# Optimization experiments

Measured on AMD Instinct MI355X. Metric: run time of the kernel, lower is better.

## Reference

```python
import jax, jax.numpy as jnp
import numpy as np

WH, WW = 7, 7
L = WH * WW            # 49 tokens per window
C = 128                # embedding dim
H = 32                 # heads
HD = C // H            # head dim = 4
BN = 4096              # batch * num_windows


def _relative_position_index(wh, ww):
    coords = np.stack(np.meshgrid(np.arange(wh), np.arange(ww), indexing='ij'))  # [2,wh,ww]
    flat = coords.reshape(2, -1)                     # [2, L]
    rel = flat[:, :, None] - flat[:, None, :]        # [2, L, L]
    rel = rel.transpose(1, 2, 0).copy()              # [L, L, 2]
    rel[:, :, 0] += wh - 1
    rel[:, :, 1] += ww - 1
    rel[:, :, 0] *= 2 * ww - 1
    return jnp.asarray(rel.sum(-1), dtype=jnp.int32)  # [L, L]


REL_IDX = _relative_position_index(WH, WW)


def setup_inputs() -> dict:
    key = jax.random.key(0)
    k1, k2, k3, k4 = jax.random.split(key, 4)
    x = jax.random.normal(k1, (BN, L, C), dtype=jnp.float32)
    W_qkv = jax.random.normal(k2, (C, 3 * C), dtype=jnp.float32) * (C ** -0.5)
    b_qkv = jnp.zeros((3 * C,), dtype=jnp.float32)
    W_proj = jax.random.normal(k3, (C, C), dtype=jnp.float32) * (C ** -0.5)
    b_proj = jnp.zeros((C,), dtype=jnp.float32)
    bias_table = jax.random.normal(k4, ((2 * WH - 1) * (2 * WW - 1), H), dtype=jnp.float32) * 0.02
    return {"x": x, "W_qkv": W_qkv, "b_qkv": b_qkv, "W_proj": W_proj,
            "b_proj": b_proj, "bias_table": bias_table}


def reference(x, W_qkv, b_qkv, W_proj, b_proj, bias_table):
    bn, l, c = x.shape
    scale = HD ** -0.5
    qkv = x @ W_qkv + b_qkv                                   # [BN, L, 3C]
    qkv = qkv.reshape(bn, l, 3, H, HD).transpose(2, 0, 3, 1, 4)  # [3, BN, H, L, HD]
    q, k, v = qkv[0], qkv[1], qkv[2]
    attn = jnp.einsum('bhqd,bhkd->bhqk', q * scale, k)        # [BN, H, L, L]
    rel_bias = bias_table[REL_IDX]                            # [L, L, H]
    attn = attn + rel_bias.transpose(2, 0, 1)[None]           # add [1, H, L, L]
    attn = jax.nn.softmax(attn, axis=-1)
    out = jnp.einsum('bhqk,bhkd->bhqd', attn, v)              # [BN, H, L, HD]
    out = out.transpose(0, 2, 1, 3).reshape(bn, l, c)         # [BN, L, C]
    return out @ W_proj + b_proj
```

## Files before the change

kernel.cpp:

```cpp
#include <hip/hip_runtime.h>
#include <hip/hip_bf16.h>
#include <stdint.h>

#define L 49
#define C 128
#define H 32

typedef __attribute__((ext_vector_type(8))) short bf16x8;
typedef __attribute__((ext_vector_type(4))) float f32x4;

#define XP 136
#define VTP 72
#define QKP 264

#define LOG2E 1.44269504f

__device__ __forceinline__ uint32_t rbits(float f) {
  return __builtin_bit_cast(uint32_t, f) + 0x8000u;
}
__device__ __forceinline__ uint32_t pack2(float a, float b) {
  return __builtin_amdgcn_perm(rbits(b), rbits(a), 0x07060302u);
}
__device__ __forceinline__ ushort bf1(float a) { return (ushort)(rbits(a) >> 16); }

__device__ __forceinline__ bf16x8 mk_frag(uint2 d, bool valid) {
  union { uint32_t u[4]; bf16x8 v; } r;
  r.u[0] = valid ? d.x : 0u;
  r.u[1] = valid ? d.y : 0u;
  r.u[2] = 0u; r.u[3] = 0u;
  return r.v;
}
__device__ __forceinline__ bf16x8 zero8() {
  union { uint32_t u[4]; bf16x8 v; } r;
  r.u[0] = r.u[1] = r.u[2] = r.u[3] = 0u;
  return r.v;
}
__device__ __forceinline__ bf16x8 ones8() {
  union { uint32_t u[4]; bf16x8 v; } r;
  r.u[0] = r.u[1] = r.u[2] = r.u[3] = 0x3F803F80u;
  return r.v;
}

__global__ void __launch_bounds__(256) prep_weights_kernel(
    const float* __restrict__ Wqkv, const float* __restrict__ Wproj,
    ushort* __restrict__ ws) {
  int i = blockIdx.x * 256 + threadIdx.x;
  if (i < 384 * 128) {
    int n = i >> 7, k = i & 127;
    ws[i] = bf1(Wqkv[k * 384 + n]);
  } else {
    int j = i - 384 * 128;
    if (j < 128 * 128) {
      int n = j >> 7, k = j & 127;
      ws[49152 + j] = bf1(Wproj[k * 128 + n]);
    }
  }
}

__global__ void __launch_bounds__(256) prep_bias_kernel(
    const float* __restrict__ bt, float* __restrict__ biasx) {
  int i = blockIdx.x * 256 + threadIdx.x;
  int r = i & 3, lane = (i >> 2) & 63, t = i >> 8;
  int nt = t & 3, mt = (t >> 2) & 3, h = t >> 4;
  int q = nt * 16 + (lane & 15);
  int k = mt * 16 + ((lane >> 4) & 3) * 4 + r;
  float v = -1e30f;
  if (q < L && k < L) {
    int qi = q / 7, qj = q % 7, ki = k / 7, kj = k % 7;
    int idx = (qi - ki + 6) * 13 + (qj - kj + 6);
    v = bt[idx * H + h] * LOG2E;
  }
  biasx[i] = v;
}

__global__ void __launch_bounds__(256, 3) win_attn_kernel(
    const float* __restrict__ x,
    const float* __restrict__ b_qkv,
    const float* __restrict__ b_proj,
    const ushort* __restrict__ wqkvT,
    const ushort* __restrict__ wprojT,
    const float* __restrict__ biasx,
    float* __restrict__ out) {
  __shared__ alignas(16) ushort s_xv[C * VTP];
  __shared__ alignas(16) ushort qk[L * QKP];
  __shared__ alignas(16) ushort p_lds[4][16 * 64];

  ushort* xa = s_xv;
  ushort* vt = s_xv;

  const int tid = threadIdx.x;
  const int w = blockIdx.x;
  const int wv = tid >> 6;
  const int l = tid & 63;
  const int lr = l & 15;
  const int lg = l >> 4;

  {
    const float4* xv = (const float4*)(x + (size_t)w * (L * C));
    for (int i = tid; i < L * C / 4; i += 256) {
      float4 v = xv[i];
      int e = i * 4;
      int r = e >> 7, c = e & 127;
      uint2 u = make_uint2(pack2(v.x, v.y), pack2(v.z, v.w));
      *(uint2*)&xa[r * XP + c] = u;
    }
  }
  __syncthreads();

  {
    bf16x8 af[4][4];
    #pragma unroll
    for (int mt = 0; mt < 4; ++mt) {
      int row = mt * 16 + lr; if (row > 48) row = 48;
      #pragma unroll
      for (int kk = 0; kk < 4; ++kk)
        af[mt][kk] = *(const bf16x8*)&xa[row * XP + kk * 32 + lg * 8];
    }
    __syncthreads();
    for (int ntl = 0; ntl < 6; ++ntl) {
      int nt = wv * 6 + ntl;
      int ncol = nt * 16 + lr;
      const ushort* bp = wqkvT + ncol * C + lg * 8;
      bf16x8 b0 = *(const bf16x8*)(bp);
      bf16x8 b1 = *(const bf16x8*)(bp + 32);
      bf16x8 b2 = *(const bf16x8*)(bp + 64);
      bf16x8 b3 = *(const bf16x8*)(bp + 96);
      float bias = b_qkv[ncol];
      float sc = (ncol < 128) ? 0.5f * LOG2E : 1.0f;
      #pragma unroll
      for (int mt = 0; mt < 4; ++mt) {
        f32x4 acc = {0.f, 0.f, 0.f, 0.f};
        acc = __builtin_amdgcn_mfma_f32_16x16x32_bf16(af[mt][0], b0, acc, 0, 0, 0);
        acc = __builtin_amdgcn_mfma_f32_16x16x32_bf16(af[mt][1], b1, acc, 0, 0, 0);
        acc = __builtin_amdgcn_mfma_f32_16x16x32_bf16(af[mt][2], b2, acc, 0, 0, 0);
        acc = __builtin_amdgcn_mfma_f32_16x16x32_bf16(af[mt][3], b3, acc, 0, 0, 0);
        if (ncol < 256) {
          #pragma unroll
          for (int r = 0; r < 4; ++r) {
            int row = mt * 16 + lg * 4 + r;
            if (row < L) qk[row * QKP + ncol] = bf1((acc[r] + bias) * sc);
          }
        } else {
          int kbase = mt * 16 + lg * 4;
          uint2 pv = make_uint2(pack2(acc[0] + bias, acc[1] + bias),
                                pack2(acc[2] + bias, acc[3] + bias));
          *(uint2*)&vt[(ncol - 256) * VTP + kbase] = pv;
        }
      }
    }
  }
  __syncthreads();

  {
    char* pw = (char*)&p_lds[wv][0];
    #pragma unroll 1
    for (int hh = 0; hh < 8; ++hh) {
      int h = wv * 8 + hh;
      f32x4 acc[4][4];
      #pragma unroll
      for (int mt = 0; mt < 4; ++mt)
        #pragma unroll
        for (int nt = 0; nt < 4; ++nt)
          acc[mt][nt] = ((const f32x4*)biasx)[(h * 16 + mt * 4 + nt) * 64 + l];
      bf16x8 ka[4], qb[4];
      #pragma unroll
      for (int mt = 0; mt < 4; ++mt) {
        int row = mt * 16 + lr; if (row > 48) row = 48;
        uint2 d = *(const uint2*)&qk[row * QKP + 128 + h * 4];
        ka[mt] = mk_frag(d, lg == 0);
      }
      #pragma unroll
      for (int nt = 0; nt < 4; ++nt) {
        int row = nt * 16 + lr; if (row > 48) row = 48;
        uint2 d = *(const uint2*)&qk[row * QKP + h * 4];
        qb[nt] = mk_frag(d, lg == 0);
      }
      #pragma unroll
      for (int nt = 0; nt < 4; ++nt)
        #pragma unroll
        for (int mt = 0; mt < 4; ++mt)
          acc[mt][nt] = __builtin_amdgcn_mfma_f32_16x16x32_bf16(ka[mt], qb[nt], acc[mt][nt], 0, 0, 0);
      bf16x8 va[2];
      #pragma unroll
      for (int ks = 0; ks < 2; ++ks) {
        bf16x8 t = *(const bf16x8*)&vt[(h * 4 + (lr & 3)) * VTP + ks * 32 + lg * 8];
        va[ks] = (lr < 4) ? t : ((lr == 4) ? ones8() : zero8());
      }
      #pragma unroll
      for (int nt = 0; nt < 4; ++nt) {
        #pragma unroll
        for (int mt = 0; mt < 4; ++mt) {
          uint32_t u0 = rbits(__builtin_amdgcn_exp2f(acc[mt][nt][0]));
          uint32_t u1 = rbits(__builtin_amdgcn_exp2f(acc[mt][nt][1]));
          uint32_t u2 = rbits(__builtin_amdgcn_exp2f(acc[mt][nt][2]));
          uint32_t u3 = rbits(__builtin_amdgcn_exp2f(acc[mt][nt][3]));
          uint32_t d0 = __builtin_amdgcn_perm(u1, u0, 0x07060302u);
          uint32_t d1 = __builtin_amdgcn_perm(u3, u2, 0x07060302u);
          int byte = lr * 128 + mt * 32 + lg * 8;
          byte ^= (lr & 7) << 4;
          *(uint2*)(pw + byte) = make_uint2(d0, d1);
        }
        f32x4 oo = {0.f, 0.f, 0.f, 0.f};
        #pragma unroll
        for (int ks = 0; ks < 2; ++ks) {
          int byte = lr * 128 + ks * 64 + lg * 16;
          byte ^= (lr & 7) << 4;
          bf16x8 pb = *(const bf16x8*)(pw + byte);
          oo = __builtin_amdgcn_mfma_f32_16x16x32_bf16(va[ks], pb, oo, 0, 0, 0);
        }
        float den = __shfl_xor(oo[0], 16);
        if (lg == 0) {
          float iv = __builtin_amdgcn_rcpf(den);
          int q = nt * 16 + lr;
          if (q < L) {
            uint2 od = make_uint2(pack2(oo[0] * iv, oo[1] * iv),
                                  pack2(oo[2] * iv, oo[3] * iv));
            *(uint2*)&qk[q * QKP + h * 4] = od;
          }
        }
      }
    }
  }
  __syncthreads();

  {
    bf16x8 pf[4][4];
    #pragma unroll
    for (int mt = 0; mt < 4; ++mt) {
      int row = mt * 16 + lr; if (row > 48) row = 48;
      #pragma unroll
      for (int kk = 0; kk < 4; ++kk)
        pf[mt][kk] = *(const bf16x8*)&qk[row * QKP + kk * 32 + lg * 8];
    }
    float* outw = out + (size_t)w * (L * C);
    for (int ntl = 0; ntl < 2; ++ntl) {
      int ncol = (wv * 2 + ntl) * 16 + lr;
      const ushort* bp = wprojT + ncol * C + lg * 8;
      bf16x8 b0 = *(const bf16x8*)(bp);
      bf16x8 b1 = *(const bf16x8*)(bp + 32);
      bf16x8 b2 = *(const bf16x8*)(bp + 64);
      bf16x8 b3 = *(const bf16x8*)(bp + 96);
      float bias = b_proj[ncol];
      #pragma unroll
      for (int mt = 0; mt < 4; ++mt) {
        f32x4 acc = {0.f, 0.f, 0.f, 0.f};
        acc = __builtin_amdgcn_mfma_f32_16x16x32_bf16(pf[mt][0], b0, acc, 0, 0, 0);
        acc = __builtin_amdgcn_mfma_f32_16x16x32_bf16(pf[mt][1], b1, acc, 0, 0, 0);
        acc = __builtin_amdgcn_mfma_f32_16x16x32_bf16(pf[mt][2], b2, acc, 0, 0, 0);
        acc = __builtin_amdgcn_mfma_f32_16x16x32_bf16(pf[mt][3], b3, acc, 0, 0, 0);
        #pragma unroll
        for (int r = 0; r < 4; ++r) {
          int row = mt * 16 + lg * 4 + r;
          if (row < L) outw[row * C + ncol] = acc[r] + bias;
        }
      }
    }
  }
}

extern "C" void kernel_launch(void* const* d_in, const int* in_sizes, int n_in,
                              void* d_out, int out_size, void* d_ws, size_t ws_size,
                              hipStream_t stream) {
  const float* x     = (const float*)d_in[0];
  const float* Wqkv  = (const float*)d_in[1];
  const float* bqkv  = (const float*)d_in[2];
  const float* Wproj = (const float*)d_in[3];
  const float* bproj = (const float*)d_in[4];
  const float* btab  = (const float*)d_in[5];
  float* out = (float*)d_out;
  ushort* ws = (ushort*)d_ws;
  float* biasx = (float*)(ws + 65536);

  int bn = in_sizes[0] / (L * C);

  hipLaunchKernelGGL(prep_weights_kernel, dim3(256), dim3(256), 0, stream,
                     Wqkv, Wproj, ws);
  hipLaunchKernelGGL(prep_bias_kernel, dim3(512), dim3(256), 0, stream,
                     btab, biasx);
  hipLaunchKernelGGL(win_attn_kernel, dim3(bn), dim3(256), 0, stream,
                     x, bqkv, bproj, ws, ws + 49152, biasx, out);
}
```

Measured before the change: 195.5 us.

## Double-buffer per-head bias loads and raise MFMA priority in attention loop

Splits the per-head attention loop into pairs of heads with two accumulator sets, so the relative-bias loads for the next head are issued while the current head computes. MFMA sections are wrapped in s_setprio to favour matrix issue across waves, and the QKV and projection column loops get an unroll-by-2 hint. The aim is to hide global bias-load latency behind compute. The second accumulator set doubles accumulator registers, which risks spills or lower occupancy under the 3-blocks-per-CU launch bound.

```diff
diff --git a/kernel.cpp b/kernel.cpp
--- a/kernel.cpp
+++ b/kernel.cpp
@@ -73,6 +73,72 @@
   biasx[i] = v;
 }
 
+__device__ __forceinline__ void head_body(
+    f32x4 (&acc)[4][4], int h, const ushort* qk, const ushort* vt,
+    char* pw, ushort* qk_mut, int lr, int lg) {
+  bf16x8 ka[4], qb[4];
+  #pragma unroll
+  for (int mt = 0; mt < 4; ++mt) {
+    int row = mt * 16 + lr; if (row > 48) row = 48;
+    uint2 d = *(const uint2*)&qk[row * QKP + 128 + h * 4];
+    ka[mt] = mk_frag(d, lg == 0);
+  }
+  #pragma unroll
+  for (int nt = 0; nt < 4; ++nt) {
+    int row = nt * 16 + lr; if (row > 48) row = 48;
+    uint2 d = *(const uint2*)&qk[row * QKP + h * 4];
+    qb[nt] = mk_frag(d, lg == 0);
+  }
+  __builtin_amdgcn_s_setprio(1);
+  #pragma unroll
+  for (int nt = 0; nt < 4; ++nt)
+    #pragma unroll
+    for (int mt = 0; mt < 4; ++mt)
+      acc[mt][nt] = __builtin_amdgcn_mfma_f32_16x16x32_bf16(ka[mt], qb[nt], acc[mt][nt], 0, 0, 0);
+  __builtin_amdgcn_s_setprio(0);
+  bf16x8 va[2];
+  #pragma unroll
+  for (int ks = 0; ks < 2; ++ks) {
+    bf16x8 t = *(const bf16x8*)&vt[(h * 4 + (lr & 3)) * VTP + ks * 32 + lg * 8];
+    va[ks] = (lr < 4) ? t : ((lr == 4) ? ones8() : zero8());
+  }
+  #pragma unroll
+  for (int nt = 0; nt < 4; ++nt) {
+    #pragma unroll
+    for (int mt = 0; mt < 4; ++mt) {
+      uint32_t u0 = rbits(__builtin_amdgcn_exp2f(acc[mt][nt][0]));
+      uint32_t u1 = rbits(__builtin_amdgcn_exp2f(acc[mt][nt][1]));
+      uint32_t u2 = rbits(__builtin_amdgcn_exp2f(acc[mt][nt][2]));
+      uint32_t u3 = rbits(__builtin_amdgcn_exp2f(acc[mt][nt][3]));
+      uint32_t d0 = __builtin_amdgcn_perm(u1, u0, 0x07060302u);
+      uint32_t d1 = __builtin_amdgcn_perm(u3, u2, 0x07060302u);
+      int byte = lr * 128 + mt * 32 + lg * 8;
+      byte ^= (lr & 7) << 4;
+      *(uint2*)(pw + byte) = make_uint2(d0, d1);
+    }
+    f32x4 oo = {0.f, 0.f, 0.f, 0.f};
+    __builtin_amdgcn_s_setprio(1);
+    #pragma unroll
+    for (int ks = 0; ks < 2; ++ks) {
+      int byte = lr * 128 + ks * 64 + lg * 16;
+      byte ^= (lr & 7) << 4;
+      bf16x8 pb = *(const bf16x8*)(pw + byte);
+      oo = __builtin_amdgcn_mfma_f32_16x16x32_bf16(va[ks], pb, oo, 0, 0, 0);
+    }
+    __builtin_amdgcn_s_setprio(0);
+    float den = __shfl_xor(oo[0], 16);
+    if (lg == 0) {
+      float iv = __builtin_amdgcn_rcpf(den);
+      int q = nt * 16 + lr;
+      if (q < L) {
+        uint2 od = make_uint2(pack2(oo[0] * iv, oo[1] * iv),
+                              pack2(oo[2] * iv, oo[3] * iv));
+        *(uint2*)&qk_mut[q * QKP + h * 4] = od;
+      }
+    }
+  }
+}
+
 __global__ void __launch_bounds__(256, 3) win_attn_kernel(
     const float* __restrict__ x,
     const float* __restrict__ b_qkv,
@@ -117,6 +183,7 @@
         af[mt][kk] = *(const bf16x8*)&xa[row * XP + kk * 32 + lg * 8];
     }
     __syncthreads();
+    #pragma unroll 2
     for (int ntl = 0; ntl < 6; ++ntl) {
       int nt = wv * 6 + ntl;
       int ncol = nt * 16 + lr;
@@ -153,72 +220,33 @@
 
   {
     char* pw = (char*)&p_lds[wv][0];
+    const f32x4* bx = (const f32x4*)biasx;
+    const int hbase = wv * 8;
+
+    f32x4 accA[4][4], accB[4][4];
+    #pragma unroll
+    for (int mt = 0; mt < 4; ++mt)
+      #pragma unroll
+      for (int nt = 0; nt < 4; ++nt)
+        accA[mt][nt] = bx[(hbase * 16 + mt * 4 + nt) * 64 + l];
+
     #pragma unroll 1
-    for (int hh = 0; hh < 8; ++hh) {
-      int h = wv * 8 + hh;
-      f32x4 acc[4][4];
+    for (int hp = 0; hp < 4; ++hp) {
+      int h0 = hbase + hp * 2;
       #pragma unroll
       for (int mt = 0; mt < 4; ++mt)
         #pragma unroll
         for (int nt = 0; nt < 4; ++nt)
-          acc[mt][nt] = ((const f32x4*)biasx)[(h * 16 + mt * 4 + nt) * 64 + l];
-      bf16x8 ka[4], qb[4];
-      #pragma unroll
-      for (int mt = 0; mt < 4; ++mt) {
-        int row = mt * 16 + lr; if (row > 48) row = 48;
-        uint2 d = *(const uint2*)&qk[row * QKP + 128 + h * 4];
-        ka[mt] = mk_frag(d, lg == 0);
-      }
-      #pragma unroll
-      for (int nt = 0; nt < 4; ++nt) {
-        int row = nt * 16 + lr; if (row > 48) row = 48;
-        uint2 d = *(const uint2*)&qk[row * QKP + h * 4];
-        qb[nt] = mk_frag(d, lg == 0);
-      }
-      #pragma unroll
-      for (int nt = 0; nt < 4; ++nt)
+          accB[mt][nt] = bx[((h0 + 1) * 16 + mt * 4 + nt) * 64 + l];
+      head_body(accA, h0, qk, vt, pw, qk, lr, lg);
+      if (hp < 3) {
         #pragma unroll
         for (int mt = 0; mt < 4; ++mt)
-          acc[mt][nt] = __builtin_amdgcn_mfma_f32_16x16x32_bf16(ka[mt], qb[nt], acc[mt][nt], 0, 0, 0);
-      bf16x8 va[2];
-      #pragma unroll
-      for (int ks = 0; ks < 2; ++ks) {
-        bf16x8 t = *(const bf16x8*)&vt[(h * 4 + (lr & 3)) * VTP + ks * 32 + lg * 8];
-        va[ks] = (lr < 4) ? t : ((lr == 4) ? ones8() : zero8());
+          #pragma unroll
+          for (int nt = 0; nt < 4; ++nt)
+            accA[mt][nt] = bx[((h0 + 2) * 16 + mt * 4 + nt) * 64 + l];
       }
-      #pragma unroll
-      for (int nt = 0; nt < 4; ++nt) {
-        #pragma unroll
-        for (int mt = 0; mt < 4; ++mt) {
-          uint32_t u0 = rbits(__builtin_amdgcn_exp2f(acc[mt][nt][0]));
-          uint32_t u1 = rbits(__builtin_amdgcn_exp2f(acc[mt][nt][1]));
-          uint32_t u2 = rbits(__builtin_amdgcn_exp2f(acc[mt][nt][2]));
-          uint32_t u3 = rbits(__builtin_amdgcn_exp2f(acc[mt][nt][3]));
-          uint32_t d0 = __builtin_amdgcn_perm(u1, u0, 0x07060302u);
-          uint32_t d1 = __builtin_amdgcn_perm(u3, u2, 0x07060302u);
-          int byte = lr * 128 + mt * 32 + lg * 8;
-          byte ^= (lr & 7) << 4;
-          *(uint2*)(pw + byte) = make_uint2(d0, d1);
-        }
-        f32x4 oo = {0.f, 0.f, 0.f, 0.f};
-        #pragma unroll
-        for (int ks = 0; ks < 2; ++ks) {
-          int byte = lr * 128 + ks * 64 + lg * 16;
-          byte ^= (lr & 7) << 4;
-          bf16x8 pb = *(const bf16x8*)(pw + byte);
-          oo = __builtin_amdgcn_mfma_f32_16x16x32_bf16(va[ks], pb, oo, 0, 0, 0);
-        }
-        float den = __shfl_xor(oo[0], 16);
-        if (lg == 0) {
-          float iv = __builtin_amdgcn_rcpf(den);
-          int q = nt * 16 + lr;
-          if (q < L) {
-            uint2 od = make_uint2(pack2(oo[0] * iv, oo[1] * iv),
-                                  pack2(oo[2] * iv, oo[3] * iv));
-            *(uint2*)&qk[q * QKP + h * 4] = od;
-          }
-        }
-      }
+      head_body(accB, h0 + 1, qk, vt, pw, qk, lr, lg);
     }
   }
   __syncthreads();
@@ -233,6 +261,7 @@
         pf[mt][kk] = *(const bf16x8*)&qk[row * QKP + kk * 32 + lg * 8];
     }
     float* outw = out + (size_t)w * (L * C);
+    #pragma unroll 2
     for (int ntl = 0; ntl < 2; ++ntl) {
       int ncol = (wv * 2 + ntl) * 16 + lr;
       const ushort* bp = wprojT + ncol * C + lg * 8;
```

New measurement: 467.0 us. +138.8%, slower.
